# Kernel tuning notes

Hardware: AMD Instinct MI355X
Metric: run time of the kernel (lower is better)

## Reference

```python
import jax, jax.numpy as jnp
import numpy as np

H = 1024      # hidden_size
NH = 16       # num_attention_heads
DK = H // NH  # head dim
C = 1024      # cyclic_size


def setup_inputs() -> dict:
    key = jax.random.key(0)
    ks = jax.random.split(key, 13)
    B, S = 2, 2048
    s = 1.0 / np.sqrt(H)
    inp = {
        "q": jax.random.normal(ks[0], (B, S, H), jnp.float32),
        "k": jax.random.normal(ks[1], (B, S, H), jnp.float32),
        "v": jax.random.normal(ks[2], (B, S, H), jnp.float32),
        "Wq": jax.random.normal(ks[3], (H, H), jnp.float32) * s,
        "bq": jnp.zeros((H,), jnp.float32),
        "Wk": jax.random.normal(ks[4], (H, H), jnp.float32) * s,
        "bk": jnp.zeros((H,), jnp.float32),
        "Wv": jax.random.normal(ks[5], (H, H), jnp.float32) * s,
        "bv": jnp.zeros((H,), jnp.float32),
        "Wo": jax.random.normal(ks[6], (H, H), jnp.float32) * s,
        "bo": jnp.zeros((H,), jnp.float32),
        "Wc": jax.random.normal(ks[7], (H, C), jnp.float32) * s,
        "bc": jnp.zeros((C,), jnp.float32),
    }
    return inp


def _split_heads(x):
    B, S, _ = x.shape
    return x.reshape(B, S, NH, DK).transpose(0, 2, 1, 3)  # [B,NH,S,DK]


def reference(q, k, v, Wq, bq, Wk, bk, Wv, bv, Wo, bo, Wc, bc):
    Q = _split_heads(q @ Wq + bq)
    K = _split_heads(k @ Wk + bk)
    V = _split_heads(v @ Wv + bv)
    # unfused SDPA: full [B,NH,S,S] scores, as in the original module
    scores = jnp.einsum("bhqd,bhkd->bhqk", Q, K) / jnp.sqrt(jnp.float32(DK))
    probs = jax.nn.softmax(scores, axis=-1)
    attn = jnp.einsum("bhqk,bhkd->bhqd", probs, V)  # [B,NH,S,DK]
    B, _, S, _ = attn.shape
    merged = attn.transpose(0, 2, 1, 3).reshape(B, S, H)
    h = merged @ Wo + bo
    c = merged @ Wc + bc
    return (c, h)
```

## Files before the change

### kernel.cpp

```cpp
#include <hip/hip_runtime.h>
#include <stdint.h>

typedef unsigned short u16;
typedef short bf16x8 __attribute__((ext_vector_type(8)));
typedef short bf16x4 __attribute__((ext_vector_type(4)));
typedef float f32x4 __attribute__((ext_vector_type(4)));

#define MB (1u<<20)
#define CL2 0.18033688f

static __device__ __forceinline__ u16 f2bf(float x){
  union { float f; unsigned u; } v; v.f = x;
  return (u16)((v.u + 0x7FFFu + ((v.u >> 16) & 1u)) >> 16);
}

static __device__ __forceinline__ void gld_lds16(const void* g, void* l){
  __builtin_amdgcn_global_load_lds((const __attribute__((address_space(1))) unsigned int*)g,
                                   (__attribute__((address_space(3))) unsigned int*)l, 16, 0, 0);
}

__global__ void convx(const float* __restrict__ q, const float* __restrict__ k, const float* __restrict__ v,
                      u16* __restrict__ qb, u16* __restrict__ kb, u16* __restrict__ vb){
  const float* s = blockIdx.z==0 ? q : (blockIdx.z==1 ? k : v);
  u16* d = blockIdx.z==0 ? qb : (blockIdx.z==1 ? kb : vb);
  int i = (blockIdx.x*256 + threadIdx.x)*4;
  float4 f = *(const float4*)(s + i);
  ushort4 o; o.x=f2bf(f.x); o.y=f2bf(f.y); o.z=f2bf(f.z); o.w=f2bf(f.w);
  *(ushort4*)(d + i) = o;
}

__global__ void convw(const float* W0,const float* W1,const float* W2,const float* W3,const float* W4,
                      u16* T0,u16* T1,u16* T2,u16* T3,u16* T4){
  const float* W = blockIdx.z==0?W0:blockIdx.z==1?W1:blockIdx.z==2?W2:blockIdx.z==3?W3:W4;
  u16* T = blockIdx.z==0?T0:blockIdx.z==1?T1:blockIdx.z==2?T2:blockIdx.z==3?T3:T4;
  __shared__ u16 t[64][65];
  int k0 = blockIdx.x*64, n0 = blockIdx.y*64;
  for (int i=0;i<16;i++){
    int idx = i*256 + threadIdx.x;
    int r = idx >> 6, c = idx & 63;
    t[r][c] = f2bf(W[(size_t)(k0+r)*1024 + n0 + c]);
  }
  __syncthreads();
  for (int i=0;i<2;i++){
    int idx = i*256 + threadIdx.x;
    int nl = idx >> 3, kc = idx & 7;
    bf16x8 o;
    #pragma unroll
    for (int j=0;j<8;j++) o[j] = (short)t[kc*8+j][nl];
    *(bf16x8*)(T + (size_t)(n0+nl)*1024 + k0 + kc*8) = o;
  }
}

template<int MODE>
static __device__ __forceinline__ void gemm_bt_dev(u16* __restrict__ As, u16* __restrict__ Bs,
                                                   const u16* __restrict__ A, const u16* __restrict__ Bt,
                                                   const float* __restrict__ bias, void* __restrict__ Cout){
  const int tid = threadIdx.x, lane = tid & 63, w = tid >> 6;
  const int wm = w >> 1, wn = w & 1, quad = lane >> 4, lr = lane & 15;
  const int fid = blockIdx.y * 8 + blockIdx.x;
  const int o   = (fid & 7) * 32 + (fid >> 3);
  const int n0  = (o & 7) * 128, m0 = (o >> 3) * 128;
  f32x4 acc[4][4] = {};
  const u16* Ab = A + (size_t)m0*1024;
  const u16* Bb = Bt + (size_t)n0*1024;
  const int srow_base = w*8 + (lane >> 3);
  const int sg = lane & 7;
  for (int k0 = 0; k0 < 1024; k0 += 64){
    #pragma unroll
    for (int j = 0; j < 4; ++j){
      int row = j*32 + srow_base;
      int g = sg ^ (row & 7);
      gld_lds16(Ab + (size_t)row*1024 + k0 + g*8, As + (j*32 + w*8)*64);
      gld_lds16(Bb + (size_t)row*1024 + k0 + g*8, Bs + (j*32 + w*8)*64);
    }
    __syncthreads();
    #pragma unroll
    for (int kk = 0; kk < 2; ++kk){
      bf16x8 af[4], bfr[4];
      #pragma unroll
      for (int i=0;i<4;i++){
        int ra = wm*64 + i*16 + lr;
        af[i]  = *(const bf16x8*)(As + ra*64 + (((kk*4+quad) ^ (ra & 7)))*8);
        int rb = wn*64 + i*16 + lr;
        bfr[i] = *(const bf16x8*)(Bs + rb*64 + (((kk*4+quad) ^ (rb & 7)))*8);
      }
      #pragma unroll
      for (int mi=0;mi<4;mi++)
        #pragma unroll
        for (int ni=0;ni<4;ni++)
          acc[mi][ni] = __builtin_amdgcn_mfma_f32_16x16x32_bf16(af[mi], bfr[ni], acc[mi][ni], 0, 0, 0);
    }
    __syncthreads();
  }
  #pragma unroll
  for (int mi=0;mi<4;mi++){
    int row = m0 + wm*64 + mi*16 + quad*4;
    #pragma unroll
    for (int ni=0;ni<4;ni++){
      int col = n0 + wn*64 + ni*16 + lr;
      float bb = bias[col];
      #pragma unroll
      for (int rg=0; rg<4; rg++){
        float vv = acc[mi][ni][rg] + bb;
        int r = row + rg;
        if (MODE == 0){
          ((u16*)Cout)[(size_t)r*1024 + col] = f2bf(vv);
        } else if (MODE == 4){
          ((u16*)Cout)[(size_t)r*1024 + col] = f2bf(vv * CL2);
        } else if (MODE == 1){
          ((float*)Cout)[(size_t)r*1024 + col] = vv;
        } else if (MODE == 2){
          int b2 = r >> 11, s = r & 2047, kb2 = s >> 7, kvl = s & 127;
          int hh = col >> 6, hg = (col & 63) >> 3, hl = col & 7;
          ((u16*)Cout)[((size_t)(b2*16+hh)*16 + kb2)*8192 + hg*1024 + kvl*8 + hl] = f2bf(vv);
        } else {
          int b2 = r >> 11, s = r & 2047, kb2 = s >> 7, kvl = s & 127;
          int sgv = kvl >> 2, sl = kvl & 3;
          int hh = col >> 6, dd = col & 63;
          ((u16*)Cout)[((size_t)(b2*16+hh)*16 + kb2)*8192 + sgv*256 + dd*4 + sl] = f2bf(vv);
        }
      }
    }
  }
}

__global__ void qkv_gemm(const u16* qb,const u16* kb,const u16* vb,
                         const u16* Wqt,const u16* Wkt,const u16* Wvt,
                         const float* bq,const float* bk,const float* bv,
                         u16* Qb,u16* Kr,u16* Vr){
  __shared__ u16 As[128*64];
  __shared__ u16 Bs[128*64];
  if (blockIdx.z == 0)      gemm_bt_dev<4>(As, Bs, qb, Wqt, bq, Qb);
  else if (blockIdx.z == 1) gemm_bt_dev<2>(As, Bs, kb, Wkt, bk, Kr);
  else                      gemm_bt_dev<3>(As, Bs, vb, Wvt, bv, Vr);
}

__global__ void out_gemm(const u16* Mg, const u16* Wct, const u16* Wot,
                         const float* bc, const float* bo, float* out){
  __shared__ u16 As[128*64];
  __shared__ u16 Bs[128*64];
  const u16* B = blockIdx.z==0? Wct : Wot;
  const float* bias = blockIdx.z==0? bc : bo;
  float* C = out + (blockIdx.z==0? 0 : 4194304);
  gemm_bt_dev<1>(As, Bs, Mg, B, bias, C);
}

__global__ __launch_bounds__(256,2) void attn(const u16* __restrict__ Qb, const u16* __restrict__ Kr,
                                              const u16* __restrict__ Vr, u16* __restrict__ Mg){
  __shared__ u16 Ks[2][8192];
  __shared__ u16 Vs[2][8192];
  const int fid = blockIdx.y * 16 + blockIdx.x;
  const int o   = (fid & 7) * 64 + (fid >> 3);
  const int qt = o & 15, bh = o >> 4, b = bh >> 4, h = bh & 15;
  const int tid = threadIdx.x, lane = tid & 63, w = tid >> 6;
  const int quad = lane >> 4, lr = lane & 15;
  const int q0 = qt*128 + w*32;

  bf16x8 aq[2][2];
  #pragma unroll
  for (int t=0;t<2;t++)
    #pragma unroll
    for (int ks=0;ks<2;ks++)
      aq[t][ks] = *(const bf16x8*)(Qb + (size_t)(b*2048 + q0 + t*16 + lr)*1024 + h*64 + ks*32 + quad*8);

  f32x4 acco[2][4] = {};
  f32x4 accl[2] = {};
  const bf16x4 ones = {(short)0x3F80,(short)0x3F80,(short)0x3F80,(short)0x3F80};

  const u16* Krb = Kr + (size_t)bh*131072;
  const u16* Vrb = Vr + (size_t)bh*131072;

  #pragma unroll
  for (int j=0;j<4;j++){
    gld_lds16(Krb + j*2048 + tid*8, &Ks[0][j*2048 + w*512]);
    gld_lds16(Vrb + j*2048 + tid*8, &Vs[0][j*2048 + w*512]);
  }

  for (int kb = 0; kb < 16; kb++){
    __syncthreads();
    const int cur = kb & 1;
    if (kb < 15){
      const u16* kg = Krb + (size_t)(kb+1)*8192;
      const u16* vg = Vrb + (size_t)(kb+1)*8192;
      #pragma unroll
      for (int j=0;j<4;j++){
        gld_lds16(kg + j*2048 + tid*8, &Ks[cur^1][j*2048 + w*512]);
        gld_lds16(vg + j*2048 + tid*8, &Vs[cur^1][j*2048 + w*512]);
      }
    }
    const u16* Ksc = Ks[cur];
    const u16* Vsc = Vs[cur];

    #pragma unroll
    for (int mt=0;mt<8;mt++){
      bf16x8 kf0 = *(const bf16x8*)(Ksc + (0*4+quad)*1024 + (mt*16+lr)*8);
      bf16x8 kf1 = *(const bf16x8*)(Ksc + (1*4+quad)*1024 + (mt*16+lr)*8);
      f32x4 a0 = {}, a1 = {};
      a0 = __builtin_amdgcn_mfma_f32_16x16x32_bf16(kf0, aq[0][0], a0, 0,0,0);
      a1 = __builtin_amdgcn_mfma_f32_16x16x32_bf16(kf0, aq[1][0], a1, 0,0,0);
      a0 = __builtin_amdgcn_mfma_f32_16x16x32_bf16(kf1, aq[0][1], a0, 0,0,0);
      a1 = __builtin_amdgcn_mfma_f32_16x16x32_bf16(kf1, aq[1][1], a1, 0,0,0);

      union { int2 i2; bf16x4 v; } pk0, pk1;
      {
        unsigned u0 = __float_as_uint(__builtin_amdgcn_exp2f(a0[0])) + 0x8000u;
        unsigned u1 = __float_as_uint(__builtin_amdgcn_exp2f(a0[1])) + 0x8000u;
        unsigned u2 = __float_as_uint(__builtin_amdgcn_exp2f(a0[2])) + 0x8000u;
        unsigned u3 = __float_as_uint(__builtin_amdgcn_exp2f(a0[3])) + 0x8000u;
        pk0.i2.x = (int)__builtin_amdgcn_perm(u1, u0, 0x07060302u);
        pk0.i2.y = (int)__builtin_amdgcn_perm(u3, u2, 0x07060302u);
      }
      {
        unsigned u0 = __float_as_uint(__builtin_amdgcn_exp2f(a1[0])) + 0x8000u;
        unsigned u1 = __float_as_uint(__builtin_amdgcn_exp2f(a1[1])) + 0x8000u;
        unsigned u2 = __float_as_uint(__builtin_amdgcn_exp2f(a1[2])) + 0x8000u;
        unsigned u3 = __float_as_uint(__builtin_amdgcn_exp2f(a1[3])) + 0x8000u;
        pk1.i2.x = (int)__builtin_amdgcn_perm(u1, u0, 0x07060302u);
        pk1.i2.y = (int)__builtin_amdgcn_perm(u3, u2, 0x07060302u);
      }

      accl[0] = __builtin_amdgcn_mfma_f32_16x16x16bf16_1k(ones, pk0.v, accl[0], 0,0,0);
      accl[1] = __builtin_amdgcn_mfma_f32_16x16x16bf16_1k(ones, pk1.v, accl[1], 0,0,0);

      #pragma unroll
      for (int dt=0;dt<4;dt++){
        bf16x4 vf = *(const bf16x4*)(Vsc + (mt*4+quad)*256 + (dt*16+lr)*4);
        acco[0][dt] = __builtin_amdgcn_mfma_f32_16x16x16bf16_1k(vf, pk0.v, acco[0][dt], 0,0,0);
        acco[1][dt] = __builtin_amdgcn_mfma_f32_16x16x16bf16_1k(vf, pk1.v, acco[1][dt], 0,0,0);
      }
    }
  }

  #pragma unroll
  for (int t=0;t<2;t++){
    float inv = 1.f / accl[t][0];
    u16* dst = Mg + (size_t)(b*2048 + q0 + t*16 + lr)*1024 + h*64;
    #pragma unroll
    for (int dt=0;dt<4;dt++){
      bf16x4 o2;
      #pragma unroll
      for (int rg=0;rg<4;rg++) o2[rg] = (short)f2bf(acco[t][dt][rg]*inv);
      *(bf16x4*)(dst + dt*16 + quad*4) = o2;
    }
  }
}

extern "C" void kernel_launch(void* const* d_in, const int* in_sizes, int n_in,
                              void* d_out, int out_size, void* d_ws, size_t ws_size,
                              hipStream_t stream){
  const float* q  = (const float*)d_in[0];
  const float* k  = (const float*)d_in[1];
  const float* v  = (const float*)d_in[2];
  const float* Wq = (const float*)d_in[3];
  const float* bq = (const float*)d_in[4];
  const float* Wk = (const float*)d_in[5];
  const float* bk = (const float*)d_in[6];
  const float* Wv = (const float*)d_in[7];
  const float* bv = (const float*)d_in[8];
  const float* Wo = (const float*)d_in[9];
  const float* bo = (const float*)d_in[10];
  const float* Wc = (const float*)d_in[11];
  const float* bc = (const float*)d_in[12];
  char* ws = (char*)d_ws;
  u16* qb  = (u16*)(ws + (size_t)0*MB);
  u16* kb  = (u16*)(ws + (size_t)8*MB);
  u16* vb  = (u16*)(ws + (size_t)16*MB);
  u16* Wqt = (u16*)(ws + (size_t)24*MB);
  u16* Wkt = (u16*)(ws + (size_t)26*MB);
  u16* Wvt = (u16*)(ws + (size_t)28*MB);
  u16* Wot = (u16*)(ws + (size_t)30*MB);
  u16* Wct = (u16*)(ws + (size_t)32*MB);
  u16* Qb  = (u16*)(ws + (size_t)34*MB);
  u16* Kr  = (u16*)(ws + (size_t)42*MB);
  u16* Vr  = (u16*)(ws + (size_t)50*MB);
  u16* Mg  = (u16*)(ws + (size_t)58*MB);

  dim3 blk(256,1,1);
  hipLaunchKernelGGL(convx,    dim3(4096,1,3), blk, 0, stream, q,k,v, qb,kb,vb);
  hipLaunchKernelGGL(convw,    dim3(16,16,5),  blk, 0, stream, Wq,Wk,Wv,Wo,Wc, Wqt,Wkt,Wvt,Wot,Wct);
  hipLaunchKernelGGL(qkv_gemm, dim3(8,32,3),   blk, 0, stream, qb,kb,vb, Wqt,Wkt,Wvt, bq,bk,bv, Qb,Kr,Vr);
  hipLaunchKernelGGL(attn,     dim3(16,32,1),  blk, 0, stream, Qb, Kr, Vr, Mg);
  hipLaunchKernelGGL(out_gemm, dim3(8,32,2),   blk, 0, stream, Mg, Wct, Wot, bc, bo, (float*)d_out);
}
```

Measured before the change: 235.9 us.

## Use 16x16x32 bf16 MFMA for PV and row-sum by pairing key tiles

The attention loop now processes two 16-key tiles per iteration and packs their exponentiated scores into one 8-wide bf16 operand. This lets the P·V and row-sum products use the K=32 MFMA instead of the K=16 one, halving those instruction counts. The V layout written by the V projection GEMM is permuted so each lane reads 8 contiguous values matching the new key pairing. In exchange it needs more live accumulator registers per iteration and depends on the producer and consumer layouts staying in sync.

```diff
diff --git a/kernel.cpp b/kernel.cpp
--- a/kernel.cpp
+++ b/kernel.cpp
@@ -17,6 +17,12 @@
 static __device__ __forceinline__ void gld_lds16(const void* g, void* l){
   __builtin_amdgcn_global_load_lds((const __attribute__((address_space(1))) unsigned int*)g,
                                    (__attribute__((address_space(3))) unsigned int*)l, 16, 0, 0);
+}
+
+static __device__ __forceinline__ int pack_bf16(float a, float b){
+  unsigned ua = __float_as_uint(a) + 0x8000u;
+  unsigned ub = __float_as_uint(b) + 0x8000u;
+  return (int)__builtin_amdgcn_perm(ub, ua, 0x07060302u);
 }
 
 __global__ void convx(const float* __restrict__ q, const float* __restrict__ k, const float* __restrict__ v,
@@ -115,9 +121,9 @@
           ((u16*)Cout)[((size_t)(b2*16+hh)*16 + kb2)*8192 + hg*1024 + kvl*8 + hl] = f2bf(vv);
         } else {
           int b2 = r >> 11, s = r & 2047, kb2 = s >> 7, kvl = s & 127;
-          int sgv = kvl >> 2, sl = kvl & 3;
+          int mt2v = kvl >> 5, gv = (kvl >> 2) & 3, jv = ((kvl >> 4) & 1)*4 + (kvl & 3);
           int hh = col >> 6, dd = col & 63;
-          ((u16*)Cout)[((size_t)(b2*16+hh)*16 + kb2)*8192 + sgv*256 + dd*4 + sl] = f2bf(vv);
+          ((u16*)Cout)[((size_t)(b2*16+hh)*16 + kb2)*8192 + (size_t)(mt2v*4+gv)*512 + dd*8 + jv] = f2bf(vv);
         }
       }
     }
@@ -165,7 +171,8 @@
 
   f32x4 acco[2][4] = {};
   f32x4 accl[2] = {};
-  const bf16x4 ones = {(short)0x3F80,(short)0x3F80,(short)0x3F80,(short)0x3F80};
+  const bf16x8 ones8 = {(short)0x3F80,(short)0x3F80,(short)0x3F80,(short)0x3F80,
+                        (short)0x3F80,(short)0x3F80,(short)0x3F80,(short)0x3F80};
 
   const u16* Krb = Kr + (size_t)bh*131072;
   const u16* Vrb = Vr + (size_t)bh*131072;
@@ -192,41 +199,43 @@
     const u16* Vsc = Vs[cur];
 
     #pragma unroll
-    for (int mt=0;mt<8;mt++){
-      bf16x8 kf0 = *(const bf16x8*)(Ksc + (0*4+quad)*1024 + (mt*16+lr)*8);
-      bf16x8 kf1 = *(const bf16x8*)(Ksc + (1*4+quad)*1024 + (mt*16+lr)*8);
-      f32x4 a0 = {}, a1 = {};
-      a0 = __builtin_amdgcn_mfma_f32_16x16x32_bf16(kf0, aq[0][0], a0, 0,0,0);
-      a1 = __builtin_amdgcn_mfma_f32_16x16x32_bf16(kf0, aq[1][0], a1, 0,0,0);
-      a0 = __builtin_amdgcn_mfma_f32_16x16x32_bf16(kf1, aq[0][1], a0, 0,0,0);
-      a1 = __builtin_amdgcn_mfma_f32_16x16x32_bf16(kf1, aq[1][1], a1, 0,0,0);
-
-      union { int2 i2; bf16x4 v; } pk0, pk1;
+    for (int mt2=0;mt2<4;mt2++){
+      f32x4 ae0 = {}, ae1 = {}, ao0 = {}, ao1 = {};
       {
-        unsigned u0 = __float_as_uint(__builtin_amdgcn_exp2f(a0[0])) + 0x8000u;
-        unsigned u1 = __float_as_uint(__builtin_amdgcn_exp2f(a0[1])) + 0x8000u;
-        unsigned u2 = __float_as_uint(__builtin_amdgcn_exp2f(a0[2])) + 0x8000u;
-        unsigned u3 = __float_as_uint(__builtin_amdgcn_exp2f(a0[3])) + 0x8000u;
-        pk0.i2.x = (int)__builtin_amdgcn_perm(u1, u0, 0x07060302u);
-        pk0.i2.y = (int)__builtin_amdgcn_perm(u3, u2, 0x07060302u);
+        bf16x8 kf0 = *(const bf16x8*)(Ksc + (0*4+quad)*1024 + ((2*mt2)*16+lr)*8);
+        bf16x8 kf1 = *(const bf16x8*)(Ksc + (1*4+quad)*1024 + ((2*mt2)*16+lr)*8);
+        ae0 = __builtin_amdgcn_mfma_f32_16x16x32_bf16(kf0, aq[0][0], ae0, 0,0,0);
+        ae1 = __builtin_amdgcn_mfma_f32_16x16x32_bf16(kf0, aq[1][0], ae1, 0,0,0);
+        ae0 = __builtin_amdgcn_mfma_f32_16x16x32_bf16(kf1, aq[0][1], ae0, 0,0,0);
+        ae1 = __builtin_amdgcn_mfma_f32_16x16x32_bf16(kf1, aq[1][1], ae1, 0,0,0);
       }
       {
-        unsigned u0 = __float_as_uint(__builtin_amdgcn_exp2f(a1[0])) + 0x8000u;
-        unsigned u1 = __float_as_uint(__builtin_amdgcn_exp2f(a1[1])) + 0x8000u;
-        unsigned u2 = __float_as_uint(__builtin_amdgcn_exp2f(a1[2])) + 0x8000u;
-        unsigned u3 = __float_as_uint(__builtin_amdgcn_exp2f(a1[3])) + 0x8000u;
-        pk1.i2.x = (int)__builtin_amdgcn_perm(u1, u0, 0x07060302u);
-        pk1.i2.y = (int)__builtin_amdgcn_perm(u3, u2, 0x07060302u);
-      }
-
-      accl[0] = __builtin_amdgcn_mfma_f32_16x16x16bf16_1k(ones, pk0.v, accl[0], 0,0,0);
-      accl[1] = __builtin_amdgcn_mfma_f32_16x16x16bf16_1k(ones, pk1.v, accl[1], 0,0,0);
+        bf16x8 kf0 = *(const bf16x8*)(Ksc + (0*4+quad)*1024 + ((2*mt2+1)*16+lr)*8);
+        bf16x8 kf1 = *(const bf16x8*)(Ksc + (1*4+quad)*1024 + ((2*mt2+1)*16+lr)*8);
+        ao0 = __builtin_amdgcn_mfma_f32_16x16x32_bf16(kf0, aq[0][0], ao0, 0,0,0);
+        ao1 = __builtin_amdgcn_mfma_f32_16x16x32_bf16(kf0, aq[1][0], ao1, 0,0,0);
+        ao0 = __builtin_amdgcn_mfma_f32_16x16x32_bf16(kf1, aq[0][1], ao0, 0,0,0);
+        ao1 = __builtin_amdgcn_mfma_f32_16x16x32_bf16(kf1, aq[1][1], ao1, 0,0,0);
+      }
+
+      union { int4 i4; bf16x8 v; } pf0, pf1;
+      pf0.i4.x = pack_bf16(__builtin_amdgcn_exp2f(ae0[0]), __builtin_amdgcn_exp2f(ae0[1]));
+      pf0.i4.y = pack_bf16(__builtin_amdgcn_exp2f(ae0[2]), __builtin_amdgcn_exp2f(ae0[3]));
+      pf0.i4.z = pack_bf16(__builtin_amdgcn_exp2f(ao0[0]), __builtin_amdgcn_exp2f(ao0[1]));
+      pf0.i4.w = pack_bf16(__builtin_amdgcn_exp2f(ao0[2]), __builtin_amdgcn_exp2f(ao0[3]));
+      pf1.i4.x = pack_bf16(__builtin_amdgcn_exp2f(ae1[0]), __builtin_amdgcn_exp2f(ae1[1]));
+      pf1.i4.y = pack_bf16(__builtin_amdgcn_exp2f(ae1[2]), __builtin_amdgcn_exp2f(ae1[3]));
+      pf1.i4.z = pack_bf16(__builtin_amdgcn_exp2f(ao1[0]), __builtin_amdgcn_exp2f(ao1[1]));
+      pf1.i4.w = pack_bf16(__builtin_amdgcn_exp2f(ao1[2]), __builtin_amdgcn_exp2f(ao1[3]));
+
+      accl[0] = __builtin_amdgcn_mfma_f32_16x16x32_bf16(ones8, pf0.v, accl[0], 0,0,0);
+      accl[1] = __builtin_amdgcn_mfma_f32_16x16x32_bf16(ones8, pf1.v, accl[1], 0,0,0);
 
       #pragma unroll
       for (int dt=0;dt<4;dt++){
-        bf16x4 vf = *(const bf16x4*)(Vsc + (mt*4+quad)*256 + (dt*16+lr)*4);
-        acco[0][dt] = __builtin_amdgcn_mfma_f32_16x16x16bf16_1k(vf, pk0.v, acco[0][dt], 0,0,0);
-        acco[1][dt] = __builtin_amdgcn_mfma_f32_16x16x16bf16_1k(vf, pk1.v, acco[1][dt], 0,0,0);
+        bf16x8 vf = *(const bf16x8*)(Vsc + (mt2*4+quad)*512 + (dt*16+lr)*8);
+        acco[0][dt] = __builtin_amdgcn_mfma_f32_16x16x32_bf16(vf, pf0.v, acco[0][dt], 0,0,0);
+        acco[1][dt] = __builtin_amdgcn_mfma_f32_16x16x32_bf16(vf, pf1.v, acco[1][dt], 0,0,0);
       }
     }
   }
```

After: 226.7 us. -3.9%, faster.
